# Optimization experiments

Hardware: AMD Instinct MI355X
Metric: run time of the kernel (lower is better)

The kernel has to match this reference:

```python
import jax, jax.numpy as jnp
import numpy as np

B, C, T = 32, 64, 1024        # batch_size, in_channels, cycle_size
H, D = 2, 64                  # GATv2 heads, per-head dim (dim_h)
DIM2 = H * D                  # dim_h * 2 = 128
K = 9                         # temporal_kernel_size
N = B * T                     # graph nodes after flatten
E = 524288                    # edges (avg degree 16)
EPS = 1e-5


def bn3d(x, gamma, beta):
    # BatchNorm1d on [B, C, T] in training mode (batch statistics)
    mu = x.mean(axis=(0, 2), keepdims=True)
    var = x.var(axis=(0, 2), keepdims=True)
    xn = (x - mu) * jax.lax.rsqrt(var + EPS)
    return xn * gamma[None, :, None] + beta[None, :, None]


def bn2d(x, gamma, beta):
    # BatchNorm1d on [N, C] in training mode
    mu = x.mean(axis=0, keepdims=True)
    var = x.var(axis=0, keepdims=True)
    return (x - mu) * jax.lax.rsqrt(var + EPS) * gamma + beta


def conv1d_same(x, w, b):
    # x: [B, Cin, T], w: [Cout, Cin, K]
    y = jax.lax.conv_general_dilated(x, w, (1,), 'SAME',
                                     dimension_numbers=('NCH', 'OIH', 'NCH'))
    return y + b[None, :, None]


def gatv2(x, edge_index, wl, wr, att, bias):
    # PyG GATv2Conv defaults: heads=H, concat=True, leaky slope 0.2, self-loops
    loops = jnp.arange(N, dtype=edge_index.dtype)
    src = jnp.concatenate([edge_index[0], loops])
    dst = jnp.concatenate([edge_index[1], loops])
    xl = (x @ wl.T).reshape(N, H, D)   # source transform
    xr = (x @ wr.T).reshape(N, H, D)   # target transform
    m = jax.nn.leaky_relu(xl[src] + xr[dst], 0.2)        # [E+N, H, D]
    logits = jnp.einsum('ehd,hd->eh', m, att)            # [E+N, H]
    lmax = jax.ops.segment_max(logits, dst, num_segments=N)
    lmax = jax.lax.stop_gradient(jnp.where(jnp.isfinite(lmax), lmax, 0.0))
    p = jnp.exp(logits - lmax[dst])
    denom = jax.ops.segment_sum(p, dst, num_segments=N)  # >0: self-loops
    alpha = p / denom[dst]                               # softmax over in-edges
    out = jax.ops.segment_sum(xl[src] * alpha[:, :, None], dst, num_segments=N)
    return out.reshape(N, DIM2) + bias


def setup_inputs() -> dict:
    key = jax.random.key(0)
    ks = jax.random.split(key, 10)
    s = lambda k, shape: jax.random.normal(k, shape, jnp.float32) * 0.05
    return {
        'x': jax.random.normal(ks[0], (B, C, T), jnp.float32),
        'edge_index': jax.random.randint(ks[1], (2, E), 0, N, jnp.int32),
        'bn0_gamma': jnp.ones((C,), jnp.float32),
        'bn0_beta': jnp.zeros((C,), jnp.float32),
        'conv_w': s(ks[2], (DIM2, C, K)),
        'conv_b': s(ks[3], (DIM2,)),
        'gat_wl': s(ks[4], (DIM2, C)),
        'gat_wr': s(ks[5], (DIM2, C)),
        'gat_att': s(ks[6], (H, D)),
        'gat_bias': s(ks[7], (DIM2,)),
        'bn1_gamma': jnp.ones((DIM2,), jnp.float32),
        'bn1_beta': jnp.zeros((DIM2,), jnp.float32),
        'cheb_w': s(ks[8], (DIM2, DIM2)),
        'cheb_b': s(ks[9], (DIM2,)),
        'train': 0,
    }


def reference(x, edge_index, bn0_gamma, bn0_beta, conv_w, conv_b,
              gat_wl, gat_wr, gat_att, gat_bias, bn1_gamma, bn1_beta,
              cheb_w, cheb_b, train):
    x = bn3d(x, bn0_gamma, bn0_beta)                       # b0 (batch_size > 1)
    residual = jax.nn.relu(conv1d_same(x, conv_w, conv_b)) # skip_connection
    h = x.reshape(T * B, C)                                # flatten to nodes
    h = gatv2(h, edge_index, gat_wl, gat_wr, gat_att, gat_bias)
    h = jax.nn.relu(bn2d(h, bn1_gamma, bn1_beta))          # b1
    h = h.reshape(B, DIM2, T)
    h = residual + h
    # chain of views: (T*B,d) -> (B,d,T) -> (B,T,-1) -> (T*B,d); pure reshapes
    h = h.reshape(T * B, DIM2)
    h = h @ cheb_w.T + cheb_b                              # ChebConv K=1 == linear
    h = jax.nn.relu(bn2d(h, bn1_gamma, bn1_beta))          # b1 again
    h = h.reshape(B, DIM2, T)
    return residual + h                                    # dropout: identity (eval)
```

## Files before the change

kernel.cpp:

```cpp
#include <hip/hip_runtime.h>

#define DEVINL __device__ __forceinline__

constexpr int Bc = 32, Cc = 64, Tc = 1024, DIM2c = 128;
constexpr int Nn = Bc * Tc;
constexpr int Ec = 524288;

typedef __bf16 bf16x8 __attribute__((ext_vector_type(8)));
typedef float  f32x4  __attribute__((ext_vector_type(4)));

constexpr long O_RES   = 0;
constexpr long O_GOUT  = 4194304;
constexpr long O_XLQ   = 10485760;
constexpr long O_XRQ   = 12582912;
constexpr long O_Z     = 16777216;
constexpr long O_WCBF  = 20971520;
constexpr long O_WLR   = 21008384;
constexpr long O_CHB   = 21016576;
constexpr long O_STAT  = 21024768;
constexpr long O_CUR   = 21025792;
constexpr long O_BUCK  = 21058560;

DEVINL float unpack_lo(unsigned v) { return __uint_as_float(v << 16); }
DEVINL float unpack_hi(unsigned v) { return __uint_as_float(v & 0xffff0000u); }
DEVINL unsigned bfb(float f) { return (__float_as_uint(f) + 0x8000u) >> 16; }
DEVINL unsigned pk2(float lo, float hi) {
    return ((__float_as_uint(hi) + 0x8000u) & 0xffff0000u) | bfb(lo);
}

__global__ __launch_bounds__(256) void setup(const float* __restrict__ x,
        const float* __restrict__ cw, const float* __restrict__ wl,
        const float* __restrict__ wr, const float* __restrict__ chw,
        const int* __restrict__ ei,
        __bf16* __restrict__ wcbf, __bf16* __restrict__ wlrbf,
        __bf16* __restrict__ chwbf,
        float* __restrict__ sum0, float* __restrict__ sq0,
        int* __restrict__ cursor, int* __restrict__ bucket) {
    int bid = blockIdx.x, tid = threadIdx.x;
    if (bid < 416) {
        int i = bid * 256 + tid;
        if (i < 73728) {
            int kk = i >> 13, co = (i >> 6) & 127, ci = i & 63;
            wcbf[i] = (__bf16)cw[co * 576 + ci * 9 + kk];
        } else if (i < 73728 + 16384) {
            int j = i - 73728;
            int r = j >> 6, c = j & 63;
            float v = (r < 128) ? wl[r * 64 + c] : wr[(r - 128) * 64 + c];
            wlrbf[j] = (__bf16)v;
        } else {
            int j = i - 73728 - 16384;
            chwbf[j] = (__bf16)chw[j];
        }
    } else if (bid < 672) {
        int pq = bid - 416;
        int c = pq & 63, q = pq >> 6;
        const float4* base = (const float4*)(x + (long)q * 8 * 65536 + (long)c * 1024);
        float s = 0.f, qq = 0.f;
        for (int i = tid; i < 2048; i += 256) {
            int b = i >> 8, t4 = i & 255;
            float4 v = base[b * 16384 + t4];
            s += v.x + v.y + v.z + v.w;
            qq = fmaf(v.x, v.x, qq); qq = fmaf(v.y, v.y, qq);
            qq = fmaf(v.z, v.z, qq); qq = fmaf(v.w, v.w, qq);
        }
        for (int off = 32; off; off >>= 1) { s += __shfl_down(s, off); qq += __shfl_down(qq, off); }
        __shared__ float ls[4], lq[4];
        int w = tid >> 6, lane = tid & 63;
        if (lane == 0) { ls[w] = s; lq[w] = qq; }
        __syncthreads();
        if (tid == 0) {
            unsafeAtomicAdd(sum0 + c, ls[0] + ls[1] + ls[2] + ls[3]);
            unsafeAtomicAdd(sq0 + c, lq[0] + lq[1] + lq[2] + lq[3]);
        }
    } else {
        int e = (bid - 672) * 256 + tid;
        int t = ei[Ec + e];
        int slot = atomicAdd(cursor + t, 1);
        bucket[t * 64 + slot] = ei[e];
    }
}

__global__ __launch_bounds__(256) void gemm1_bn0(const float* __restrict__ x,
        const float* __restrict__ sum0, const float* __restrict__ sq0,
        const float* __restrict__ g0, const float* __restrict__ b0,
        const __bf16* __restrict__ wlrbf,
        unsigned short* __restrict__ xl16, unsigned short* __restrict__ xr16) {
    __shared__ __align__(16) __bf16 as_[64 * 72];
    int tid = threadIdx.x;
    int mb = blockIdx.x;
    int b = mb >> 4, ci0 = (mb & 15) * 4;
    const float4* x4 = (const float4*)(x + (long)b * 65536 + (long)ci0 * 1024);
    #pragma unroll
    for (int it = 0; it < 4; it++) {
        int ci = ci0 + it;
        float mu = sum0[ci] * (1.f / 32768.f);
        float var = sq0[ci] * (1.f / 32768.f) - mu * mu;
        float sc = rsqrtf(var + 1e-5f) * g0[ci];
        float sh = b0[ci] - mu * sc;
        float4 v = x4[it * 256 + tid];
        int row = it * 16 + (tid >> 4);
        int col = (tid & 15) * 4;
        __bf16* p = as_ + row * 72 + col;
        p[0] = (__bf16)fmaf(v.x, sc, sh);
        p[1] = (__bf16)fmaf(v.y, sc, sh);
        p[2] = (__bf16)fmaf(v.z, sc, sh);
        p[3] = (__bf16)fmaf(v.w, sc, sh);
    }
    __syncthreads();
    int wv = tid >> 6, lane = tid & 63;
    int col = lane & 15, q = lane >> 4;
    int d0 = wv * 16;
    long mbase = (long)mb * 64;
    bf16x8 bfr[4][2];
    #pragma unroll
    for (int t = 0; t < 4; t++) {
        int j = d0 + t * 64 + col;
        #pragma unroll
        for (int ks = 0; ks < 2; ks++)
            bfr[t][ks] = *(const bf16x8*)(wlrbf + (long)j * 64 + ks * 32 + q * 8);
    }
    int d = d0 + col;
    for (int mt = 0; mt < 4; mt++) {
        const __bf16* ap = as_ + (mt * 16 + col) * 72;
        bf16x8 a0 = *(const bf16x8*)(ap + q * 8);
        bf16x8 a1 = *(const bf16x8*)(ap + 32 + q * 8);
        f32x4 acc[4];
        #pragma unroll
        for (int t = 0; t < 4; t++) { acc[t][0] = 0.f; acc[t][1] = 0.f; acc[t][2] = 0.f; acc[t][3] = 0.f; }
        #pragma unroll
        for (int t = 0; t < 4; t++) {
            acc[t] = __builtin_amdgcn_mfma_f32_16x16x32_bf16(a0, bfr[t][0], acc[t], 0, 0, 0);
            acc[t] = __builtin_amdgcn_mfma_f32_16x16x32_bf16(a1, bfr[t][1], acc[t], 0, 0, 0);
        }
        long r0 = mbase + mt * 16;
        #pragma unroll
        for (int reg = 0; reg < 4; reg++) {
            long rb = (r0 + q * 4 + reg) * 128;
            xl16[rb + d]      = (unsigned short)bfb(acc[0][reg]);
            xl16[rb + 64 + d] = (unsigned short)bfb(acc[1][reg]);
            xr16[rb + d]      = (unsigned short)bfb(acc[2][reg]);
            xr16[rb + 64 + d] = (unsigned short)bfb(acc[3][reg]);
        }
    }
}

constexpr int XS_STRIDE = 72;

DEVINL void conv_role(int cid, const float* __restrict__ x,
        const float* __restrict__ sum0, const float* __restrict__ sq0,
        const float* __restrict__ g0, const float* __restrict__ b0,
        const __bf16* __restrict__ wcbf, const float* __restrict__ cb,
        float* __restrict__ res, __bf16* xs, float* scs, float* shs) {
    int tid = threadIdx.x;
    int tbase = (cid & 7) * 128;
    int cohalf = (cid >> 3) & 1;
    int b = cid >> 4;
    if (tid < 64) {
        float mu = sum0[tid] * (1.f / 32768.f);
        float var = sq0[tid] * (1.f / 32768.f) - mu * mu;
        float sc = rsqrtf(var + 1e-5f) * g0[tid];
        scs[tid] = sc; shs[tid] = b0[tid] - mu * sc;
    }
    __syncthreads();
    int w = tid >> 6, lane = tid & 63;
    const float* xb = x + (long)b * 65536;
    for (int cc = 0; cc < 16; cc++) {
        int ci = w * 16 + cc;
        float sc = scs[ci], sh = shs[ci];
        const float* xp = xb + ci * 1024 + tbase - 4;
        #pragma unroll
        for (int rp = 0; rp < 2; rp++) {
            int rr = rp * 64 + lane;
            int t = tbase - 4 + rr;
            float v = 0.f;
            if ((unsigned)t < 1024u) v = fmaf(xp[rr], sc, sh);
            xs[rr * XS_STRIDE + ci] = (__bf16)v;
        }
        if (lane < 8) {
            int rr = 128 + lane;
            int t = tbase - 4 + rr;
            float v = 0.f;
            if ((unsigned)t < 1024u) v = fmaf(xp[rr], sc, sh);
            xs[rr * XS_STRIDE + ci] = (__bf16)v;
        }
    }
    __syncthreads();
    int col = lane & 15, q = lane >> 4;
    int co0 = cohalf * 64 + w * 16;
    bf16x8 af[18];
    #pragma unroll
    for (int kk = 0; kk < 9; kk++)
        #pragma unroll
        for (int ks = 0; ks < 2; ks++)
            af[kk * 2 + ks] = *(const bf16x8*)(wcbf +
                ((long)kk * 8192 + (long)(co0 + col) * 64 + ks * 32 + q * 8));
    float bi0 = cb[co0 + q * 4], bi1 = cb[co0 + q * 4 + 1];
    float bi2 = cb[co0 + q * 4 + 2], bi3 = cb[co0 + q * 4 + 3];
    for (int nt = 0; nt < 8; nt++) {
        int t0 = tbase + nt * 16;
        f32x4 acc; acc[0] = bi0; acc[1] = bi1; acc[2] = bi2; acc[3] = bi3;
        #pragma unroll
        for (int kk = 0; kk < 9; kk++) {
            const __bf16* rp = xs + (nt * 16 + col + kk) * XS_STRIDE + q * 8;
            #pragma unroll
            for (int ks = 0; ks < 2; ks++) {
                bf16x8 bfx = *(const bf16x8*)(rp + ks * 32);
                acc = __builtin_amdgcn_mfma_f32_16x16x32_bf16(af[kk * 2 + ks], bfx, acc, 0, 0, 0);
            }
        }
        long ob = (long)b * 131072 + (long)(co0 + q * 4) * 1024 + t0 + col;
        res[ob]        = fmaxf(acc[0], 0.f);
        res[ob + 1024] = fmaxf(acc[1], 0.f);
        res[ob + 2048] = fmaxf(acc[2], 0.f);
        res[ob + 3072] = fmaxf(acc[3], 0.f);
    }
}

DEVINL void gat_role(int wid, const uint4* __restrict__ xlq4,
        const uint4* __restrict__ xrq4,
        const int* __restrict__ cursor, const int* __restrict__ bucket,
        const float* __restrict__ att, unsigned* __restrict__ goutb) {
    int lane = threadIdx.x & 63;
    int g = lane >> 3, j = lane & 7;
    float av[16];
    #pragma unroll
    for (int k = 0; k < 16; k++) av[k] = att[16 * j + k];
    uint4 r0v = xrq4[(long)wid * 16 + j * 2];
    uint4 r1v = xrq4[(long)wid * 16 + j * 2 + 1];
    float xr[16];
    {
        unsigned ru[8] = {r0v.x, r0v.y, r0v.z, r0v.w, r1v.x, r1v.y, r1v.z, r1v.w};
        #pragma unroll
        for (int k = 0; k < 8; k++) { xr[2*k] = unpack_lo(ru[k]); xr[2*k+1] = unpack_hi(ru[k]); }
    }
    int cnt = cursor[wid];
    int s_all = bucket[wid * 64 + lane];
    float acc[16];
    #pragma unroll
    for (int k = 0; k < 16; k++) acc[k] = 0.f;
    float den = 0.f;
    int nit = (cnt + 8) >> 3;
    int sp = __shfl(s_all, g);
    sp = (g < cnt) ? sp : wid;
    uint4 p0 = xlq4[(long)sp * 16 + j * 2];
    uint4 p1 = xlq4[(long)sp * 16 + j * 2 + 1];
    for (int it = 0; it < nit; it++) {
        uint4 c0 = p0, c1 = p1;
        int icur = it * 8 + g;
        int inext = icur + 8;
        if (it + 1 < nit) {
            int sn = __shfl(s_all, inext & 63);
            sn = (inext < cnt) ? sn : wid;
            p0 = xlq4[(long)sn * 16 + j * 2];
            p1 = xlq4[(long)sn * 16 + j * 2 + 1];
        }
        unsigned uu[8] = {c0.x, c0.y, c0.z, c0.w, c1.x, c1.y, c1.z, c1.w};
        float xl[16];
        float w = 0.f;
        #pragma unroll
        for (int k = 0; k < 8; k++) {
            float lo = unpack_lo(uu[k]), hi = unpack_hi(uu[k]);
            xl[2*k] = lo; xl[2*k+1] = hi;
            float s0 = lo + xr[2*k]; s0 = fmaxf(s0, 0.2f * s0);
            float s1 = hi + xr[2*k+1]; s1 = fmaxf(s1, 0.2f * s1);
            w = fmaf(s1, av[2*k+1], fmaf(s0, av[2*k], w));
        }
        w += __shfl_xor(w, 1); w += __shfl_xor(w, 2);
        float e2 = (icur <= cnt) ? __expf(w) : 0.f;
        den += e2;
        #pragma unroll
        for (int k = 0; k < 16; k++) acc[k] = fmaf(e2, xl[k], acc[k]);
    }
    #pragma unroll
    for (int m = 8; m <= 32; m <<= 1) {
        den += __shfl_xor(den, m);
        #pragma unroll
        for (int k = 0; k < 16; k++) acc[k] += __shfl_xor(acc[k], m);
    }
    float rn = __builtin_amdgcn_rcpf(den);
    if (g == 0) {
        #pragma unroll
        for (int c = 0; c < 2; c++) {
            uint4 o;
            o.x = pk2(acc[8*c]     * rn, acc[8*c + 1] * rn);
            o.y = pk2(acc[8*c + 2] * rn, acc[8*c + 3] * rn);
            o.z = pk2(acc[8*c + 4] * rn, acc[8*c + 5] * rn);
            o.w = pk2(acc[8*c + 6] * rn, acc[8*c + 7] * rn);
            *(uint4*)(goutb + (long)wid * 64 + 8 * j + 4 * c) = o;
        }
    }
}

__global__ __launch_bounds__(256) void conv_gat(const float* __restrict__ x,
        const float* __restrict__ sum0, const float* __restrict__ sq0,
        const float* __restrict__ g0, const float* __restrict__ b0,
        const __bf16* __restrict__ wcbf, const float* __restrict__ cb,
        float* __restrict__ res,
        const uint4* __restrict__ xlq4, const uint4* __restrict__ xrq4,
        const int* __restrict__ cursor, const int* __restrict__ bucket,
        const float* __restrict__ att, unsigned* __restrict__ goutb) {
    __shared__ __align__(16) __bf16 xs[136 * XS_STRIDE];
    __shared__ float scs[64], shs[64];
    int bid = blockIdx.x;
    if (bid < 512)
        conv_role(bid, x, sum0, sq0, g0, b0, wcbf, cb, res, xs, scs, shs);
    else
        gat_role(((bid - 512) * 256 + (int)threadIdx.x) >> 6,
                 xlq4, xrq4, cursor, bucket, att, goutb);
}

__global__ __launch_bounds__(256) void bn_stats_bf(const unsigned* __restrict__ G,
        float* __restrict__ sum, float* __restrict__ sq) {
    int c = threadIdx.x & 63, sub = threadIdx.x >> 6;
    int r0 = blockIdx.x * 128;
    float sl = 0.f, sh = 0.f, ql = 0.f, qh = 0.f;
    for (int r = r0 + sub; r < r0 + 128; r += 4) {
        unsigned v = G[(long)r * 64 + c];
        float lo = unpack_lo(v), hi = unpack_hi(v);
        sl += lo; ql = fmaf(lo, lo, ql);
        sh += hi; qh = fmaf(hi, hi, qh);
    }
    __shared__ float A[256], B[256], C[256], D[256];
    A[threadIdx.x] = sl; B[threadIdx.x] = sh;
    C[threadIdx.x] = ql; D[threadIdx.x] = qh;
    __syncthreads();
    if (threadIdx.x < 64) {
        int t = threadIdx.x;
        float s_lo = A[t] + A[t + 64] + A[t + 128] + A[t + 192];
        float s_hi = B[t] + B[t + 64] + B[t + 128] + B[t + 192];
        float q_lo = C[t] + C[t + 64] + C[t + 128] + C[t + 192];
        float q_hi = D[t] + D[t + 64] + D[t + 128] + D[t + 192];
        unsafeAtomicAdd(sum + 2 * t,     s_lo);
        unsafeAtomicAdd(sum + 2 * t + 1, s_hi);
        unsafeAtomicAdd(sq  + 2 * t,     q_lo);
        unsafeAtomicAdd(sq  + 2 * t + 1, q_hi);
    }
}

__global__ __launch_bounds__(256) void cheb_fused(const unsigned* __restrict__ goutb,
        const float* __restrict__ res, const float* __restrict__ sum1,
        const float* __restrict__ sq1, const float* __restrict__ g1,
        const float* __restrict__ b1, const __bf16* __restrict__ chwbf,
        unsigned* __restrict__ zb, float* __restrict__ sum2, float* __restrict__ sq2) {
    __shared__ unsigned xsu[64 * 68];
    __shared__ float scs[128], shs[128], cs[128], cq[128];
    int tid = threadIdx.x;
    if (tid < 128) {
        float mu = sum1[tid] * (1.f / 32768.f);
        float var = sq1[tid] * (1.f / 32768.f) - mu * mu;
        float rs = rsqrtf(var + 1e-5f);
        float sc = rs * g1[tid];
        scs[tid] = sc; shs[tid] = b1[tid] - mu * sc;
        cs[tid] = 0.f;
    } else cq[tid - 128] = 0.f;
    __syncthreads();
    long r0 = (long)blockIdx.x * 64;
    for (int i = tid; i < 2048; i += 256) {
        int row = i >> 5, c4 = i & 31;
        long gidx = (r0 + row) * 32 + c4;
        uint2 gv = ((const uint2*)goutb)[gidx];
        float4 r = ((const float4*)res)[gidx];
        int f0 = c4 * 4;
        float v0 = unpack_lo(gv.x), v1 = unpack_hi(gv.x);
        float v2 = unpack_lo(gv.y), v3 = unpack_hi(gv.y);
        float o0 = r.x + fmaxf(fmaf(v0, scs[f0],     shs[f0]),     0.f);
        float o1 = r.y + fmaxf(fmaf(v1, scs[f0 + 1], shs[f0 + 1]), 0.f);
        float o2 = r.z + fmaxf(fmaf(v2, scs[f0 + 2], shs[f0 + 2]), 0.f);
        float o3 = r.w + fmaxf(fmaf(v3, scs[f0 + 3], shs[f0 + 3]), 0.f);
        xsu[row * 68 + c4 * 2]     = pk2(o0, o1);
        xsu[row * 68 + c4 * 2 + 1] = pk2(o2, o3);
    }
    __syncthreads();
    int wv = tid >> 6, lane = tid & 63;
    int col = lane & 15, q = lane >> 4;
    bf16x8 bfr[2][4];
    #pragma unroll
    for (int t = 0; t < 2; t++) {
        int jj = wv * 16 + t * 64 + col;
        #pragma unroll
        for (int ks = 0; ks < 4; ks++)
            bfr[t][ks] = *(const bf16x8*)(chwbf + (long)jj * 128 + ks * 32 + q * 8);
    }
    float ls0 = 0.f, ls1 = 0.f, lq0 = 0.f, lq1 = 0.f;
    bool evenc = (col & 1) == 0;
    int fpair0 = (wv * 16 + col) >> 1;
    for (int mt = 0; mt < 4; mt++) {
        const __bf16* ap = (const __bf16*)xsu + (mt * 16 + col) * 136;
        bf16x8 a[4];
        #pragma unroll
        for (int ks = 0; ks < 4; ks++)
            a[ks] = *(const bf16x8*)(ap + ks * 32 + q * 8);
        f32x4 acc[2];
        #pragma unroll
        for (int t = 0; t < 2; t++) { acc[t][0] = 0.f; acc[t][1] = 0.f; acc[t][2] = 0.f; acc[t][3] = 0.f; }
        #pragma unroll
        for (int t = 0; t < 2; t++)
            #pragma unroll
            for (int ks = 0; ks < 4; ks++)
                acc[t] = __builtin_amdgcn_mfma_f32_16x16x32_bf16(a[ks], bfr[t][ks], acc[t], 0, 0, 0);
        #pragma unroll
        for (int reg = 0; reg < 4; reg++) {
            float v0 = acc[0][reg], v1 = acc[1][reg];
            ls0 += v0; lq0 = fmaf(v0, v0, lq0);
            ls1 += v1; lq1 = fmaf(v1, v1, lq1);
            float n0 = __shfl_xor(v0, 1);
            float n1 = __shfl_xor(v1, 1);
            if (evenc) {
                long zrow = (r0 + mt * 16 + q * 4 + reg) * 64;
                zb[zrow + fpair0]      = pk2(v0, n0);
                zb[zrow + 32 + fpair0] = pk2(v1, n1);
            }
        }
    }
    int j0 = wv * 16 + col;
    atomicAdd(&cs[j0], ls0);      atomicAdd(&cs[j0 + 64], ls1);
    atomicAdd(&cq[j0], lq0);      atomicAdd(&cq[j0 + 64], lq1);
    __syncthreads();
    if (tid < 128) unsafeAtomicAdd(sum2 + tid, cs[tid]);
    else unsafeAtomicAdd(sq2 + tid - 128, cq[tid - 128]);
}

__global__ __launch_bounds__(256) void bn_res(const unsigned* __restrict__ zb,
        const float* __restrict__ res, const float* __restrict__ sum,
        const float* __restrict__ sq, const float* __restrict__ g,
        const float* __restrict__ bta, float* __restrict__ out) {
    __shared__ float scs[128], shs[128];
    int tid = threadIdx.x;
    if (tid < 128) {
        float mu = sum[tid] * (1.f / 32768.f);
        float var = sq[tid] * (1.f / 32768.f) - mu * mu;
        float rs = rsqrtf(var + 1e-5f);
        float sc = rs * g[tid];
        scs[tid] = sc; shs[tid] = bta[tid] - mu * sc;
    }
    __syncthreads();
    int idx = blockIdx.x * 256 + tid;
    int f0 = (idx & 31) * 4;
    uint2 zv = ((const uint2*)zb)[idx];
    float4 r = ((const float4*)res)[idx];
    float v0 = unpack_lo(zv.x), v1 = unpack_hi(zv.x);
    float v2 = unpack_lo(zv.y), v3 = unpack_hi(zv.y);
    float4 o;
    o.x = r.x + fmaxf(fmaf(v0, scs[f0],     shs[f0]),     0.f);
    o.y = r.y + fmaxf(fmaf(v1, scs[f0 + 1], shs[f0 + 1]), 0.f);
    o.z = r.z + fmaxf(fmaf(v2, scs[f0 + 2], shs[f0 + 2]), 0.f);
    o.w = r.w + fmaxf(fmaf(v3, scs[f0 + 3], shs[f0 + 3]), 0.f);
    ((float4*)out)[idx] = o;
}

extern "C" void kernel_launch(void* const* d_in, const int* in_sizes, int n_in,
                              void* d_out, int out_size, void* d_ws, size_t ws_size,
                              hipStream_t stream) {
    const float* x   = (const float*)d_in[0];
    const int*   ei  = (const int*)d_in[1];
    const float* g0  = (const float*)d_in[2];
    const float* b0  = (const float*)d_in[3];
    const float* cw  = (const float*)d_in[4];
    const float* cb  = (const float*)d_in[5];
    const float* wl  = (const float*)d_in[6];
    const float* wr  = (const float*)d_in[7];
    const float* att = (const float*)d_in[8];
    const float* g1  = (const float*)d_in[10];
    const float* b1  = (const float*)d_in[11];
    const float* chw = (const float*)d_in[12];
    float* out = (float*)d_out;

    float* ws = (float*)d_ws;
    float*    res   = ws + O_RES;
    unsigned* goutb = (unsigned*)(ws + O_GOUT);
    unsigned* xlq   = (unsigned*)(ws + O_XLQ);
    unsigned* xrq   = (unsigned*)(ws + O_XRQ);
    unsigned* zb    = (unsigned*)(ws + O_Z);
    __bf16*   wcbf  = (__bf16*)(ws + O_WCBF);
    __bf16*   wlrbf = (__bf16*)(ws + O_WLR);
    __bf16*   chwbf = (__bf16*)(ws + O_CHB);
    float*    st    = ws + O_STAT;
    int*      cursor = (int*)(ws + O_CUR);
    int*      bucket = (int*)(ws + O_BUCK);
    float *sum0 = st,       *sq0 = st + 64;
    float *sum1 = st + 128, *sq1 = st + 256;
    float *sum2 = st + 384, *sq2 = st + 512;

    hipMemsetAsync(st, 0, (size_t)(1024 + 32768) * 4, stream);

    setup<<<2720, 256, 0, stream>>>(x, cw, wl, wr, chw, ei,
                                    wcbf, wlrbf, chwbf, sum0, sq0, cursor, bucket);
    gemm1_bn0<<<512, 256, 0, stream>>>(x, sum0, sq0, g0, b0, wlrbf,
                                       (unsigned short*)xlq, (unsigned short*)xrq);
    conv_gat<<<8704, 256, 0, stream>>>(x, sum0, sq0, g0, b0, wcbf, cb, res,
                                       (const uint4*)xlq, (const uint4*)xrq,
                                       cursor, bucket, att, goutb);
    bn_stats_bf<<<256, 256, 0, stream>>>(goutb, sum1, sq1);
    cheb_fused<<<512, 256, 0, stream>>>(goutb, res, sum1, sq1, g1, b1, chwbf,
                                        zb, sum2, sq2);
    bn_res<<<4096, 256, 0, stream>>>(zb, res, sum2, sq2, g1, b1, out);
}
```

Measured before the change: 219.2 us.

## Move edge bucketing into gemm1 launch, widen GAT lanes per edge, reorder roles

Edge bucketing moves out of the setup kernel and into the same launch as the xl/xr GEMM as extra blocks, so setup becomes shorter and bucketing overlaps with the GEMM. The GAT role now maps 16 lanes per edge with one uint4 each, so 4 edges are processed per iteration with a two-deep prefetch, in place of 8 lanes with two uint4 each and 8 edges per iteration. This halves per-lane registers and increases the number of loads in flight. In the fused conv/GAT launch, GAT blocks are scheduled before conv blocks. The risks are more loop iterations for high-degree nodes, an extra shuffle step in the reduction, and a changed tail balance.

After: 227.8 us. 3.9% more time.

```diff
diff --git a/kernel.cpp b/kernel.cpp
--- a/kernel.cpp
+++ b/kernel.cpp
@@ -31,11 +31,9 @@
 __global__ __launch_bounds__(256) void setup(const float* __restrict__ x,
         const float* __restrict__ cw, const float* __restrict__ wl,
         const float* __restrict__ wr, const float* __restrict__ chw,
-        const int* __restrict__ ei,
         __bf16* __restrict__ wcbf, __bf16* __restrict__ wlrbf,
         __bf16* __restrict__ chwbf,
-        float* __restrict__ sum0, float* __restrict__ sq0,
-        int* __restrict__ cursor, int* __restrict__ bucket) {
+        float* __restrict__ sum0, float* __restrict__ sq0) {
     int bid = blockIdx.x, tid = threadIdx.x;
     if (bid < 416) {
         int i = bid * 256 + tid;
@@ -51,7 +49,7 @@
             int j = i - 73728 - 16384;
             chwbf[j] = (__bf16)chw[j];
         }
-    } else if (bid < 672) {
+    } else {
         int pq = bid - 416;
         int c = pq & 63, q = pq >> 6;
         const float4* base = (const float4*)(x + (long)q * 8 * 65536 + (long)c * 1024);
@@ -72,22 +70,16 @@
             unsafeAtomicAdd(sum0 + c, ls[0] + ls[1] + ls[2] + ls[3]);
             unsafeAtomicAdd(sq0 + c, lq[0] + lq[1] + lq[2] + lq[3]);
         }
-    } else {
-        int e = (bid - 672) * 256 + tid;
-        int t = ei[Ec + e];
-        int slot = atomicAdd(cursor + t, 1);
-        bucket[t * 64 + slot] = ei[e];
-    }
-}
-
-__global__ __launch_bounds__(256) void gemm1_bn0(const float* __restrict__ x,
+    }
+}
+
+DEVINL void gemm1_body(int mb, const float* __restrict__ x,
         const float* __restrict__ sum0, const float* __restrict__ sq0,
         const float* __restrict__ g0, const float* __restrict__ b0,
         const __bf16* __restrict__ wlrbf,
-        unsigned short* __restrict__ xl16, unsigned short* __restrict__ xr16) {
-    __shared__ __align__(16) __bf16 as_[64 * 72];
+        unsigned short* __restrict__ xl16, unsigned short* __restrict__ xr16,
+        __bf16* as_) {
     int tid = threadIdx.x;
-    int mb = blockIdx.x;
     int b = mb >> 4, ci0 = (mb & 15) * 4;
     const float4* x4 = (const float4*)(x + (long)b * 65536 + (long)ci0 * 1024);
     #pragma unroll
@@ -144,6 +136,25 @@
     }
 }
 
+__global__ __launch_bounds__(256) void gemm1_bucket(const float* __restrict__ x,
+        const float* __restrict__ sum0, const float* __restrict__ sq0,
+        const float* __restrict__ g0, const float* __restrict__ b0,
+        const __bf16* __restrict__ wlrbf,
+        unsigned short* __restrict__ xl16, unsigned short* __restrict__ xr16,
+        const int* __restrict__ ei, int* __restrict__ cursor,
+        int* __restrict__ bucket) {
+    __shared__ __align__(16) __bf16 as_[64 * 72];
+    int bid = blockIdx.x;
+    if (bid < 2048) {
+        int e = bid * 256 + threadIdx.x;
+        int t = ei[Ec + e];
+        int slot = atomicAdd(cursor + t, 1);
+        bucket[t * 64 + slot] = ei[e];
+    } else {
+        gemm1_body(bid - 2048, x, sum0, sq0, g0, b0, wlrbf, xl16, xr16, as_);
+    }
+}
+
 constexpr int XS_STRIDE = 72;
 
 DEVINL void conv_role(int cid, const float* __restrict__ x,
@@ -221,73 +232,75 @@
         const int* __restrict__ cursor, const int* __restrict__ bucket,
         const float* __restrict__ att, unsigned* __restrict__ goutb) {
     int lane = threadIdx.x & 63;
-    int g = lane >> 3, j = lane & 7;
-    float av[16];
-    #pragma unroll
-    for (int k = 0; k < 16; k++) av[k] = att[16 * j + k];
-    uint4 r0v = xrq4[(long)wid * 16 + j * 2];
-    uint4 r1v = xrq4[(long)wid * 16 + j * 2 + 1];
-    float xr[16];
+    int g = lane >> 4, j = lane & 15;
+    const float4* att4 = (const float4*)att;
+    float4 a0 = att4[2 * j], a1 = att4[2 * j + 1];
+    float av[8] = {a0.x, a0.y, a0.z, a0.w, a1.x, a1.y, a1.z, a1.w};
+    uint4 rv = xrq4[(long)wid * 16 + j];
+    float xr[8];
     {
-        unsigned ru[8] = {r0v.x, r0v.y, r0v.z, r0v.w, r1v.x, r1v.y, r1v.z, r1v.w};
-        #pragma unroll
-        for (int k = 0; k < 8; k++) { xr[2*k] = unpack_lo(ru[k]); xr[2*k+1] = unpack_hi(ru[k]); }
+        unsigned ru[4] = {rv.x, rv.y, rv.z, rv.w};
+        #pragma unroll
+        for (int k = 0; k < 4; k++) { xr[2*k] = unpack_lo(ru[k]); xr[2*k+1] = unpack_hi(ru[k]); }
     }
     int cnt = cursor[wid];
     int s_all = bucket[wid * 64 + lane];
-    float acc[16];
+    float acc[8];
     #pragma unroll
-    for (int k = 0; k < 16; k++) acc[k] = 0.f;
+    for (int k = 0; k < 8; k++) acc[k] = 0.f;
     float den = 0.f;
-    int nit = (cnt + 8) >> 3;
-    int sp = __shfl(s_all, g);
-    sp = (g < cnt) ? sp : wid;
-    uint4 p0 = xlq4[(long)sp * 16 + j * 2];
-    uint4 p1 = xlq4[(long)sp * 16 + j * 2 + 1];
+    int nit = (cnt + 4) >> 2;
+    int i0 = g;
+    int sp = __shfl(s_all, i0);
+    sp = (i0 < cnt) ? sp : wid;
+    uint4 p0 = xlq4[(long)sp * 16 + j];
+    uint4 p1; p1.x = 0u; p1.y = 0u; p1.z = 0u; p1.w = 0u;
+    if (nit > 1) {
+        int i1 = 4 + g;
+        int s1 = __shfl(s_all, i1);
+        s1 = (i1 < cnt) ? s1 : wid;
+        p1 = xlq4[(long)s1 * 16 + j];
+    }
     for (int it = 0; it < nit; it++) {
-        uint4 c0 = p0, c1 = p1;
-        int icur = it * 8 + g;
-        int inext = icur + 8;
-        if (it + 1 < nit) {
-            int sn = __shfl(s_all, inext & 63);
-            sn = (inext < cnt) ? sn : wid;
-            p0 = xlq4[(long)sn * 16 + j * 2];
-            p1 = xlq4[(long)sn * 16 + j * 2 + 1];
-        }
-        unsigned uu[8] = {c0.x, c0.y, c0.z, c0.w, c1.x, c1.y, c1.z, c1.w};
-        float xl[16];
+        uint4 c = p0; p0 = p1;
+        int icur = it * 4 + g;
+        int inx = icur + 8;
+        if (it + 2 < nit) {
+            int sn = __shfl(s_all, inx & 63);
+            sn = (inx < cnt) ? sn : wid;
+            p1 = xlq4[(long)sn * 16 + j];
+        }
+        unsigned uu[4] = {c.x, c.y, c.z, c.w};
+        float xl[8];
         float w = 0.f;
         #pragma unroll
-        for (int k = 0; k < 8; k++) {
+        for (int k = 0; k < 4; k++) {
             float lo = unpack_lo(uu[k]), hi = unpack_hi(uu[k]);
             xl[2*k] = lo; xl[2*k+1] = hi;
             float s0 = lo + xr[2*k]; s0 = fmaxf(s0, 0.2f * s0);
             float s1 = hi + xr[2*k+1]; s1 = fmaxf(s1, 0.2f * s1);
             w = fmaf(s1, av[2*k+1], fmaf(s0, av[2*k], w));
         }
-        w += __shfl_xor(w, 1); w += __shfl_xor(w, 2);
+        w += __shfl_xor(w, 1); w += __shfl_xor(w, 2); w += __shfl_xor(w, 4);
         float e2 = (icur <= cnt) ? __expf(w) : 0.f;
         den += e2;
         #pragma unroll
-        for (int k = 0; k < 16; k++) acc[k] = fmaf(e2, xl[k], acc[k]);
+        for (int k = 0; k < 8; k++) acc[k] = fmaf(e2, xl[k], acc[k]);
     }
     #pragma unroll
-    for (int m = 8; m <= 32; m <<= 1) {
+    for (int m = 16; m <= 32; m <<= 1) {
         den += __shfl_xor(den, m);
         #pragma unroll
-        for (int k = 0; k < 16; k++) acc[k] += __shfl_xor(acc[k], m);
+        for (int k = 0; k < 8; k++) acc[k] += __shfl_xor(acc[k], m);
     }
     float rn = __builtin_amdgcn_rcpf(den);
     if (g == 0) {
-        #pragma unroll
-        for (int c = 0; c < 2; c++) {
-            uint4 o;
-            o.x = pk2(acc[8*c]     * rn, acc[8*c + 1] * rn);
-            o.y = pk2(acc[8*c + 2] * rn, acc[8*c + 3] * rn);
-            o.z = pk2(acc[8*c + 4] * rn, acc[8*c + 5] * rn);
-            o.w = pk2(acc[8*c + 6] * rn, acc[8*c + 7] * rn);
-            *(uint4*)(goutb + (long)wid * 64 + 8 * j + 4 * c) = o;
-        }
+        uint4 o;
+        o.x = pk2(acc[0] * rn, acc[1] * rn);
+        o.y = pk2(acc[2] * rn, acc[3] * rn);
+        o.z = pk2(acc[4] * rn, acc[5] * rn);
+        o.w = pk2(acc[6] * rn, acc[7] * rn);
+        *(uint4*)(goutb + (long)wid * 64 + 4 * j) = o;
     }
 }
 
@@ -302,11 +315,11 @@
     __shared__ __align__(16) __bf16 xs[136 * XS_STRIDE];
     __shared__ float scs[64], shs[64];
     int bid = blockIdx.x;
-    if (bid < 512)
-        conv_role(bid, x, sum0, sq0, g0, b0, wcbf, cb, res, xs, scs, shs);
+    if (bid < 8192)
+        gat_role((bid * 256 + (int)threadIdx.x) >> 6,
+                 xlq4, xrq4, cursor, bucket, att, goutb);
     else
-        gat_role(((bid - 512) * 256 + (int)threadIdx.x) >> 6,
-                 xlq4, xrq4, cursor, bucket, att, goutb);
+        conv_role(bid - 8192, x, sum0, sq0, g0, b0, wcbf, cb, res, xs, scs, shs);
 }
 
 __global__ __launch_bounds__(256) void bn_stats_bf(const unsigned* __restrict__ G,
@@ -483,10 +496,11 @@
 
     hipMemsetAsync(st, 0, (size_t)(1024 + 32768) * 4, stream);
 
-    setup<<<2720, 256, 0, stream>>>(x, cw, wl, wr, chw, ei,
-                                    wcbf, wlrbf, chwbf, sum0, sq0, cursor, bucket);
-    gemm1_bn0<<<512, 256, 0, stream>>>(x, sum0, sq0, g0, b0, wlrbf,
-                                       (unsigned short*)xlq, (unsigned short*)xrq);
+    setup<<<672, 256, 0, stream>>>(x, cw, wl, wr, chw,
+                                   wcbf, wlrbf, chwbf, sum0, sq0);
+    gemm1_bucket<<<2560, 256, 0, stream>>>(x, sum0, sq0, g0, b0, wlrbf,
+                                           (unsigned short*)xlq, (unsigned short*)xrq,
+                                           ei, cursor, bucket);
     conv_gat<<<8704, 256, 0, stream>>>(x, sum0, sq0, g0, b0, wcbf, cb, res,
                                        (const uint4*)xlq, (const uint4*)xrq,
                                        cursor, bucket, att, goutb);
```

## Move edge bucketing into gemm1 launch and deepen GAT gather prefetch

Applied to the files above, without the earlier changes.

The edge bucketing (atomic scatter of sources by destination) moves out of the setup kernel and into a combined launch with the xl/xr projection GEMM. Setup becomes short, and the bucketing blocks run alongside the GEMM blocks. Separately, the GAT aggregation loop now prefetches neighbour features two iterations ahead instead of one, hiding more gather latency at the cost of extra registers. The combined kernel carries the GEMM's shared memory footprint for every block, including the bucket blocks that don't use it.

Result: slower. 228.1 us (+4.1%).

```diff
diff --git a/kernel.cpp b/kernel.cpp
--- a/kernel.cpp
+++ b/kernel.cpp
@@ -31,11 +31,9 @@
 __global__ __launch_bounds__(256) void setup(const float* __restrict__ x,
         const float* __restrict__ cw, const float* __restrict__ wl,
         const float* __restrict__ wr, const float* __restrict__ chw,
-        const int* __restrict__ ei,
         __bf16* __restrict__ wcbf, __bf16* __restrict__ wlrbf,
         __bf16* __restrict__ chwbf,
-        float* __restrict__ sum0, float* __restrict__ sq0,
-        int* __restrict__ cursor, int* __restrict__ bucket) {
+        float* __restrict__ sum0, float* __restrict__ sq0) {
     int bid = blockIdx.x, tid = threadIdx.x;
     if (bid < 416) {
         int i = bid * 256 + tid;
@@ -51,7 +49,7 @@
             int j = i - 73728 - 16384;
             chwbf[j] = (__bf16)chw[j];
         }
-    } else if (bid < 672) {
+    } else {
         int pq = bid - 416;
         int c = pq & 63, q = pq >> 6;
         const float4* base = (const float4*)(x + (long)q * 8 * 65536 + (long)c * 1024);
@@ -72,22 +70,16 @@
             unsafeAtomicAdd(sum0 + c, ls[0] + ls[1] + ls[2] + ls[3]);
             unsafeAtomicAdd(sq0 + c, lq[0] + lq[1] + lq[2] + lq[3]);
         }
-    } else {
-        int e = (bid - 672) * 256 + tid;
-        int t = ei[Ec + e];
-        int slot = atomicAdd(cursor + t, 1);
-        bucket[t * 64 + slot] = ei[e];
-    }
-}
-
-__global__ __launch_bounds__(256) void gemm1_bn0(const float* __restrict__ x,
+    }
+}
+
+DEVINL void gemm1_body(int mb, const float* __restrict__ x,
         const float* __restrict__ sum0, const float* __restrict__ sq0,
         const float* __restrict__ g0, const float* __restrict__ b0,
         const __bf16* __restrict__ wlrbf,
-        unsigned short* __restrict__ xl16, unsigned short* __restrict__ xr16) {
-    __shared__ __align__(16) __bf16 as_[64 * 72];
+        unsigned short* __restrict__ xl16, unsigned short* __restrict__ xr16,
+        __bf16* as_) {
     int tid = threadIdx.x;
-    int mb = blockIdx.x;
     int b = mb >> 4, ci0 = (mb & 15) * 4;
     const float4* x4 = (const float4*)(x + (long)b * 65536 + (long)ci0 * 1024);
     #pragma unroll
@@ -144,6 +136,25 @@
     }
 }
 
+__global__ __launch_bounds__(256) void gemm1_bucket(const float* __restrict__ x,
+        const float* __restrict__ sum0, const float* __restrict__ sq0,
+        const float* __restrict__ g0, const float* __restrict__ b0,
+        const __bf16* __restrict__ wlrbf,
+        unsigned short* __restrict__ xl16, unsigned short* __restrict__ xr16,
+        const int* __restrict__ ei, int* __restrict__ cursor,
+        int* __restrict__ bucket) {
+    __shared__ __align__(16) __bf16 as_[64 * 72];
+    int bid = blockIdx.x;
+    if (bid < 2048) {
+        int e = bid * 256 + threadIdx.x;
+        int t = ei[Ec + e];
+        int slot = atomicAdd(cursor + t, 1);
+        bucket[t * 64 + slot] = ei[e];
+    } else {
+        gemm1_body(bid - 2048, x, sum0, sq0, g0, b0, wlrbf, xl16, xr16, as_);
+    }
+}
+
 constexpr int XS_STRIDE = 72;
 
 DEVINL void conv_role(int cid, const float* __restrict__ x,
@@ -244,15 +255,24 @@
     sp = (g < cnt) ? sp : wid;
     uint4 p0 = xlq4[(long)sp * 16 + j * 2];
     uint4 p1 = xlq4[(long)sp * 16 + j * 2 + 1];
+    uint4 q0 = p0, q1 = p1;
+    if (nit > 1) {
+        int i1 = 8 + g;
+        int s1 = __shfl(s_all, i1);
+        s1 = (i1 < cnt) ? s1 : wid;
+        q0 = xlq4[(long)s1 * 16 + j * 2];
+        q1 = xlq4[(long)s1 * 16 + j * 2 + 1];
+    }
     for (int it = 0; it < nit; it++) {
         uint4 c0 = p0, c1 = p1;
+        p0 = q0; p1 = q1;
         int icur = it * 8 + g;
-        int inext = icur + 8;
-        if (it + 1 < nit) {
-            int sn = __shfl(s_all, inext & 63);
-            sn = (inext < cnt) ? sn : wid;
-            p0 = xlq4[(long)sn * 16 + j * 2];
-            p1 = xlq4[(long)sn * 16 + j * 2 + 1];
+        int inx = icur + 16;
+        if (it + 2 < nit) {
+            int sn = __shfl(s_all, inx & 63);
+            sn = (inx < cnt) ? sn : wid;
+            q0 = xlq4[(long)sn * 16 + j * 2];
+            q1 = xlq4[(long)sn * 16 + j * 2 + 1];
         }
         unsigned uu[8] = {c0.x, c0.y, c0.z, c0.w, c1.x, c1.y, c1.z, c1.w};
         float xl[16];
@@ -483,10 +503,11 @@
 
     hipMemsetAsync(st, 0, (size_t)(1024 + 32768) * 4, stream);
 
-    setup<<<2720, 256, 0, stream>>>(x, cw, wl, wr, chw, ei,
-                                    wcbf, wlrbf, chwbf, sum0, sq0, cursor, bucket);
-    gemm1_bn0<<<512, 256, 0, stream>>>(x, sum0, sq0, g0, b0, wlrbf,
-                                       (unsigned short*)xlq, (unsigned short*)xrq);
+    setup<<<672, 256, 0, stream>>>(x, cw, wl, wr, chw,
+                                   wcbf, wlrbf, chwbf, sum0, sq0);
+    gemm1_bucket<<<2560, 256, 0, stream>>>(x, sum0, sq0, g0, b0, wlrbf,
+                                           (unsigned short*)xlq, (unsigned short*)xrq,
+                                           ei, cursor, bucket);
     conv_gat<<<8704, 256, 0, stream>>>(x, sum0, sq0, g0, b0, wcbf, cb, res,
                                        (const uint4*)xlq, (const uint4*)xrq,
                                        cursor, bucket, att, goutb);
```

## Map one GAT node per 8-lane group instead of one node per wavefront

Applied to the files above, without the earlier changes.

The GATv2 aggregation role now gives each 8-lane group its own destination node, so a wavefront handles 8 nodes instead of 1. Each group walks its node's in-edges one at a time and loops up to the wavefront's maximum in-degree. This removes the cross-group shuffle reduction and cuts the GAT grid from 8192 to 1024 blocks. The trade-off is divergence: groups whose nodes have fewer edges sit idle while the wavefront finishes the busiest node, and the serial per-edge loop has less memory-level parallelism per node.

New measurement: 221.1 us. No clear change (+0.9%).

```diff
diff --git a/kernel.cpp b/kernel.cpp
--- a/kernel.cpp
+++ b/kernel.cpp
@@ -216,41 +216,44 @@
     }
 }
 
-DEVINL void gat_role(int wid, const uint4* __restrict__ xlq4,
+DEVINL void gat_role(int wvid, const uint4* __restrict__ xlq4,
         const uint4* __restrict__ xrq4,
         const int* __restrict__ cursor, const int* __restrict__ bucket,
         const float* __restrict__ att, unsigned* __restrict__ goutb) {
     int lane = threadIdx.x & 63;
     int g = lane >> 3, j = lane & 7;
+    int n = wvid * 8 + g;
     float av[16];
     #pragma unroll
     for (int k = 0; k < 16; k++) av[k] = att[16 * j + k];
-    uint4 r0v = xrq4[(long)wid * 16 + j * 2];
-    uint4 r1v = xrq4[(long)wid * 16 + j * 2 + 1];
+    uint4 r0v = xrq4[(long)n * 16 + j * 2];
+    uint4 r1v = xrq4[(long)n * 16 + j * 2 + 1];
     float xr[16];
     {
         unsigned ru[8] = {r0v.x, r0v.y, r0v.z, r0v.w, r1v.x, r1v.y, r1v.z, r1v.w};
         #pragma unroll
         for (int k = 0; k < 8; k++) { xr[2*k] = unpack_lo(ru[k]); xr[2*k+1] = unpack_hi(ru[k]); }
     }
-    int cnt = cursor[wid];
-    int s_all = bucket[wid * 64 + lane];
+    int cnt = cursor[n];
+    const int* bk = bucket + (long)n * 64;
+    int mx = cnt;
+    mx = max(mx, __shfl_xor(mx, 8));
+    mx = max(mx, __shfl_xor(mx, 16));
+    mx = max(mx, __shfl_xor(mx, 32));
     float acc[16];
     #pragma unroll
     for (int k = 0; k < 16; k++) acc[k] = 0.f;
     float den = 0.f;
-    int nit = (cnt + 8) >> 3;
-    int sp = __shfl(s_all, g);
-    sp = (g < cnt) ? sp : wid;
-    uint4 p0 = xlq4[(long)sp * 16 + j * 2];
-    uint4 p1 = xlq4[(long)sp * 16 + j * 2 + 1];
-    for (int it = 0; it < nit; it++) {
+    int s0 = (0 < cnt) ? bk[0] : n;
+    uint4 p0 = xlq4[(long)s0 * 16 + j * 2];
+    uint4 p1 = xlq4[(long)s0 * 16 + j * 2 + 1];
+    int s_next = (1 < cnt) ? bk[1] : n;
+    for (int it = 0; it <= mx; it++) {
         uint4 c0 = p0, c1 = p1;
-        int icur = it * 8 + g;
-        int inext = icur + 8;
-        if (it + 1 < nit) {
-            int sn = __shfl(s_all, inext & 63);
-            sn = (inext < cnt) ? sn : wid;
+        int sn = s_next;
+        int i2 = it + 2;
+        s_next = (i2 < cnt) ? bk[i2] : n;
+        if (it < mx) {
             p0 = xlq4[(long)sn * 16 + j * 2];
             p1 = xlq4[(long)sn * 16 + j * 2 + 1];
         }
@@ -261,34 +264,28 @@
         for (int k = 0; k < 8; k++) {
             float lo = unpack_lo(uu[k]), hi = unpack_hi(uu[k]);
             xl[2*k] = lo; xl[2*k+1] = hi;
-            float s0 = lo + xr[2*k]; s0 = fmaxf(s0, 0.2f * s0);
-            float s1 = hi + xr[2*k+1]; s1 = fmaxf(s1, 0.2f * s1);
-            w = fmaf(s1, av[2*k+1], fmaf(s0, av[2*k], w));
+            float s0f = lo + xr[2*k]; s0f = fmaxf(s0f, 0.2f * s0f);
+            float s1f = hi + xr[2*k+1]; s1f = fmaxf(s1f, 0.2f * s1f);
+            w = fmaf(s1f, av[2*k+1], fmaf(s0f, av[2*k], w));
         }
         w += __shfl_xor(w, 1); w += __shfl_xor(w, 2);
-        float e2 = (icur <= cnt) ? __expf(w) : 0.f;
+        float e2 = (it <= cnt) ? __expf(w) : 0.f;
         den += e2;
         #pragma unroll
         for (int k = 0; k < 16; k++) acc[k] = fmaf(e2, xl[k], acc[k]);
     }
-    #pragma unroll
-    for (int m = 8; m <= 32; m <<= 1) {
-        den += __shfl_xor(den, m);
-        #pragma unroll
-        for (int k = 0; k < 16; k++) acc[k] += __shfl_xor(acc[k], m);
-    }
     float rn = __builtin_amdgcn_rcpf(den);
-    if (g == 0) {
-        #pragma unroll
-        for (int c = 0; c < 2; c++) {
-            uint4 o;
-            o.x = pk2(acc[8*c]     * rn, acc[8*c + 1] * rn);
-            o.y = pk2(acc[8*c + 2] * rn, acc[8*c + 3] * rn);
-            o.z = pk2(acc[8*c + 4] * rn, acc[8*c + 5] * rn);
-            o.w = pk2(acc[8*c + 6] * rn, acc[8*c + 7] * rn);
-            *(uint4*)(goutb + (long)wid * 64 + 8 * j + 4 * c) = o;
-        }
-    }
+    uint4 o0, o1;
+    o0.x = pk2(acc[0] * rn, acc[1] * rn);
+    o0.y = pk2(acc[2] * rn, acc[3] * rn);
+    o0.z = pk2(acc[4] * rn, acc[5] * rn);
+    o0.w = pk2(acc[6] * rn, acc[7] * rn);
+    o1.x = pk2(acc[8] * rn, acc[9] * rn);
+    o1.y = pk2(acc[10] * rn, acc[11] * rn);
+    o1.z = pk2(acc[12] * rn, acc[13] * rn);
+    o1.w = pk2(acc[14] * rn, acc[15] * rn);
+    *(uint4*)(goutb + (long)n * 64 + 8 * j)     = o0;
+    *(uint4*)(goutb + (long)n * 64 + 8 * j + 4) = o1;
 }
 
 __global__ __launch_bounds__(256) void conv_gat(const float* __restrict__ x,
@@ -305,7 +302,7 @@
     if (bid < 512)
         conv_role(bid, x, sum0, sq0, g0, b0, wcbf, cb, res, xs, scs, shs);
     else
-        gat_role(((bid - 512) * 256 + (int)threadIdx.x) >> 6,
+        gat_role((bid - 512) * 4 + ((int)threadIdx.x >> 6),
                  xlq4, xrq4, cursor, bucket, att, goutb);
 }
 
@@ -487,7 +484,7 @@
                                     wcbf, wlrbf, chwbf, sum0, sq0, cursor, bucket);
     gemm1_bn0<<<512, 256, 0, stream>>>(x, sum0, sq0, g0, b0, wlrbf,
                                        (unsigned short*)xlq, (unsigned short*)xrq);
-    conv_gat<<<8704, 256, 0, stream>>>(x, sum0, sq0, g0, b0, wcbf, cb, res,
+    conv_gat<<<1536, 256, 0, stream>>>(x, sum0, sq0, g0, b0, wcbf, cb, res,
                                        (const uint4*)xlq, (const uint4*)xrq,
                                        cursor, bucket, att, goutb);
     bn_stats_bf<<<256, 256, 0, stream>>>(goutb, sum1, sq1);
```
